# Optimization experiments

Hardware: AMD Instinct MI355X
Metric: run time of the kernel (lower is better)

## Reference

```python
import jax, jax.numpy as jnp
import numpy as np

B, N, K, IN_CH = 512, 64, 16, 6   # graphs, nodes per graph, knn, input features
EPS = 1e-5


def _w(key, shape, fan_in):
    return jax.random.normal(key, shape, jnp.float32) / np.sqrt(fan_in)


def setup_inputs() -> dict:
    key = jax.random.key(0)
    ks = jax.random.split(key, 16)
    f32 = jnp.float32
    inp = {
        "x": jax.random.normal(ks[0], (B * N, IN_CH), f32),
        "batch": (jnp.arange(B * N, dtype=jnp.int32) // N).astype(jnp.int32),
        # input projection 6 -> 64
        "w_in": _w(ks[1], (IN_CH, 64), IN_CH), "g_in": jnp.ones(64, f32), "b_in": jnp.zeros(64, f32),
        # ec1: SharedMLP([128, 64, 64])
        "w1a": _w(ks[2], (128, 64), 128), "g1a": jnp.ones(64, f32), "b1a": jnp.zeros(64, f32),
        "w1b": _w(ks[3], (64, 64), 64),   "g1b": jnp.ones(64, f32), "b1b": jnp.zeros(64, f32),
        # ec2: SharedMLP([128, 128, 128])
        "w2a": _w(ks[4], (128, 128), 128), "g2a": jnp.ones(128, f32), "b2a": jnp.zeros(128, f32),
        "w2b": _w(ks[5], (128, 128), 128), "g2b": jnp.ones(128, f32), "b2b": jnp.zeros(128, f32),
        # ec3: SharedMLP([256, 256, 256])
        "w3a": _w(ks[6], (256, 256), 256), "g3a": jnp.ones(256, f32), "b3a": jnp.zeros(256, f32),
        "w3b": _w(ks[7], (256, 256), 256), "g3b": jnp.ones(256, f32), "b3b": jnp.zeros(256, f32),
        # classifier head (dropout is identity in eval mode)
        "wc1": _w(ks[8], (896, 512), 896), "gc1": jnp.ones(512, f32), "bc1": jnp.zeros(512, f32),
        "wc2": _w(ks[9], (512, 256), 512), "gc2": jnp.ones(256, f32), "bc2": jnp.zeros(256, f32),
        "wc3": _w(ks[10], (256, 2), 256),  "bc3": jnp.zeros(2, f32),
    }
    return inp


def bn(h, g, b):
    # training-mode BatchNorm1d over all leading (node/edge) dims, biased var
    ax = tuple(range(h.ndim - 1))
    m = h.mean(ax)
    v = h.var(ax)
    return g * (h - m) * jax.lax.rsqrt(v + EPS) + b


def lrelu(h):
    return jax.nn.leaky_relu(h, 0.2)


def knn(x):
    # x: [B,N,C]; per-graph squared-Euclidean kNN (excluding self)
    sq = jnp.sum(x * x, -1)
    d = sq[:, :, None] - 2.0 * jnp.einsum('bnc,bmc->bnm', x, x) + sq[:, None, :]
    _, idx = jax.lax.top_k(-d, K + 1)  # K+1 smallest distances
    return idx[:, :, 1:]               # drop self -> [B,N,K]


def edge_conv(x, w1, g1, b1, w2, g2, b2):
    # Dynamic EdgeConv, aggr='max'. Edge (src=centre c, dst=neighbour n):
    # target x_i = x_n, message = MLP(cat[x_i, x_j - x_i]) with x_j = x_c.
    idx = knn(x)                                     # [B,N,K]
    xn = jax.vmap(lambda xb, ib: xb[ib])(x, idx)     # [B,N,K,C] neighbours
    xc = x[:, :, None, :]                            # centres broadcast
    feat = jnp.concatenate([xn, xc - xn], -1)        # [B,N,K,2C]
    h = lrelu(bn(feat @ w1, g1, b1))
    h = lrelu(bn(h @ w2, g2, b2))                    # [B,N,K,Cout]
    C = h.shape[-1]

    def scatter_max(ib, hb):  # per-graph max-scatter to destination nodes
        out = jnp.full((N, C), -jnp.inf, hb.dtype)
        return out.at[ib.reshape(-1)].max(hb.reshape(-1, C))

    res = jax.vmap(scatter_max)(idx, h)
    return jnp.where(jnp.isneginf(res), 0.0, res)    # nodes w/o in-edges -> 0


def reference(x, batch, w_in, g_in, b_in,
              w1a, g1a, b1a, w1b, g1b, b1b,
              w2a, g2a, b2a, w2b, g2b, b2b,
              w3a, g3a, b3a, w3b, g3b, b3b,
              wc1, gc1, bc1, wc2, gc2, bc2, wc3, bc3):
    # batch == arange(B*N)//N (equal-size graphs), encoded by the [B,N] reshape
    h0 = lrelu(bn(x @ w_in, g_in, b_in)).reshape(B, N, 64)
    h1 = edge_conv(h0, w1a, g1a, b1a, w1b, g1b, b1b)   # [B,N,64]
    h2 = edge_conv(h1, w2a, g2a, b2a, w2b, g2b, b2b)   # [B,N,128]
    h3 = edge_conv(h2, w3a, g3a, b3a, w3b, g3b, b3b)   # [B,N,256]
    h = jnp.concatenate([h1, h2, h3], -1)              # [B,N,448]
    pooled = jnp.concatenate([h.mean(1), h.max(1)], -1)  # [B,896]
    z = lrelu(bn(pooled @ wc1, gc1, bc1))
    z = lrelu(bn(z @ wc2, gc2, bc2))
    return z @ wc3 + bc3                               # [B,2] logits
```

## Files before the change

kernel.cpp:

```cpp
#include <hip/hip_runtime.h>
#include <hip/hip_fp16.h>
#include <math.h>

#define BB 512
#define NN 64
#define KNB 16
#define NPTS (BB*NN)
#define NEDGE (BB*NN*KNB)
#define EPSV 1e-5f

typedef __attribute__((ext_vector_type(8))) _Float16 f16x8;
typedef __attribute__((ext_vector_type(4))) _Float16 f16x4;
typedef __attribute__((ext_vector_type(4))) float f32x4;

__device__ __forceinline__ float lrelu(float x){ return fmaxf(x, 0.2f*x); }
__device__ __forceinline__ unsigned encf(float f){
    unsigned u = __float_as_uint(f);
    return (u & 0x80000000u) ? ~u : (u | 0x80000000u);
}
__device__ __forceinline__ float decf(unsigned e){
    unsigned u = (e & 0x80000000u) ? (e ^ 0x80000000u) : ~e;
    return __uint_as_float(u);
}
#define ENC_NEGINF 0x007FFFFFu

__device__ __forceinline__ float dec_ec(unsigned e, float ca, float cb, float gv){
    if (e == ENC_NEGINF) return 0.0f;
    float s = (gv < 0.0f) ? -1.0f : 1.0f;
    return lrelu(ca*(s*decf(e)) + cb);
}

__device__ __forceinline__ void split2h(float v, _Float16& h, _Float16& m){
    h = (_Float16)v;
    float r = v - (float)h;
    m = (_Float16)(r * 2048.0f);
}

__global__ void k_input(const float* __restrict__ x, const float* __restrict__ w,
                        float* __restrict__ h0){
    __shared__ float wls[6*64];
    int t = threadIdx.x;
    for (int i = t; i < 6*64; i += 256) wls[i] = w[i];
    __syncthreads();
    int row = blockIdx.x*256 + t;
    float xv[6];
#pragma unroll
    for (int k = 0; k < 6; k++) xv[k] = x[row*6 + k];
#pragma unroll 8
    for (int c = 0; c < 64; c++){
        float acc = 0.f;
#pragma unroll
        for (int k = 0; k < 6; k++) acc += xv[k]*wls[k*64 + c];
        h0[(size_t)row*64 + c] = acc;
    }
}

__global__ void k_colstats_part(const float* __restrict__ h,
                                float* __restrict__ pS, float* __restrict__ pQ){
    int t = threadIdx.x;
    int c = t & 63;
    int g = t >> 6;
    int p = blockIdx.x*4 + g;
    const int rpb = NPTS/256;
    int r0 = p*rpb;
    float s = 0.f, q = 0.f;
    for (int r = r0; r < r0 + rpb; r++){
        float v = h[(size_t)r*64 + c];
        s += v; q += v*v;
    }
    pS[c*256 + p] = s;
    pQ[c*256 + p] = q;
}

__global__ void k_bnfin_part(const float* __restrict__ pS, const float* __restrict__ pQ,
                             const float* __restrict__ g, const float* __restrict__ b,
                             float* __restrict__ cA, float* __restrict__ cB,
                             int P, float invM){
    int c = threadIdx.x;
    const float* ps = pS + (size_t)c*P;
    const float* pq = pQ + (size_t)c*P;
    float s = 0.f, q = 0.f;
    for (int p = 0; p < P; p += 4){
        float4 vs = *(const float4*)(ps + p);
        float4 vq = *(const float4*)(pq + p);
        s += vs.x + vs.y + vs.z + vs.w;
        q += vq.x + vq.y + vq.z + vq.w;
    }
    float m = s*invM;
    float v = q*invM - m*m;
    v = v < 0.f ? 0.f : v;
    float a = g[c]*rsqrtf(v + EPSV);
    cA[c] = a;
    cB[c] = b[c] - m*a;
}

__global__ void k_bnfin(const float* gs, const float* gq, const float* g,
                        const float* b, float* cA, float* cB, int C, float invM){
    int c = blockIdx.x*blockDim.x + threadIdx.x;
    if (c < C){
        float m = gs[c]*invM;
        float v = gq[c]*invM - m*m;
        v = v < 0.f ? 0.f : v;
        float a = g[c]*rsqrtf(v + EPSV);
        cA[c] = a;
        cB[c] = b[c] - m*a;
    }
}

template<int C, int MODE>
__global__ void k_knn(const void* __restrict__ xin, int* __restrict__ idxg,
                      const float* __restrict__ cA, const float* __restrict__ cB,
                      const float* __restrict__ g){
    const int CP = C + 4;
    __shared__ __align__(16) float xls[64*CP];
    __shared__ float sq[64];
    __shared__ __align__(16) float dls[64*64];
    int t = threadIdx.x, b = blockIdx.x;
    if (MODE == 0){
        const float* xb = (const float*)xin + (size_t)b*64*C;
        for (int i = t; i < 64*C; i += 256){
            int n = i / C, c = i & (C-1);
            xls[n*CP + c] = lrelu(cA[c]*xb[i] + cB[c]);
        }
    } else {
        const unsigned* xb = (const unsigned*)xin + (size_t)b*64*C;
        for (int i = t; i < 64*C; i += 256){
            int n = i / C, c = i & (C-1);
            xls[n*CP + c] = dec_ec(xb[i], cA[c], cB[c], g[c]);
        }
    }
    __syncthreads();
    if (t < 64){
        float s = 0.f;
        for (int c = 0; c < C; c += 4){
            float4 v = *(const float4*)&xls[t*CP + c];
            s += v.x*v.x + v.y*v.y + v.z*v.z + v.w*v.w;
        }
        sq[t] = s;
    }
    __syncthreads();
    {
        int n0 = (t >> 3)*2;
        int m0 = (t & 7)*8;
        float acc[2][8];
#pragma unroll
        for (int r = 0; r < 2; r++)
#pragma unroll
            for (int i = 0; i < 8; i++) acc[r][i] = 0.f;
        const float* an0 = &xls[n0*CP];
        const float* an1 = &xls[(n0+1)*CP];
        const float* bm  = &xls[m0*CP];
        for (int c = 0; c < C; c += 4){
            float4 a0 = *(const float4*)(an0 + c);
            float4 a1 = *(const float4*)(an1 + c);
#pragma unroll
            for (int i = 0; i < 8; i++){
                float4 bv = *(const float4*)(bm + i*CP + c);
                acc[0][i] += a0.x*bv.x + a0.y*bv.y + a0.z*bv.z + a0.w*bv.w;
                acc[1][i] += a1.x*bv.x + a1.y*bv.y + a1.z*bv.z + a1.w*bv.w;
            }
        }
#pragma unroll
        for (int r = 0; r < 2; r++){
            float sn = sq[n0 + r];
#pragma unroll
            for (int i4 = 0; i4 < 8; i4 += 4){
                float4 dv;
                dv.x = sn - 2.0f*acc[r][i4+0] + sq[m0+i4+0];
                dv.y = sn - 2.0f*acc[r][i4+1] + sq[m0+i4+1];
                dv.z = sn - 2.0f*acc[r][i4+2] + sq[m0+i4+2];
                dv.w = sn - 2.0f*acc[r][i4+3] + sq[m0+i4+3];
                *(float4*)&dls[(n0+r)*64 + m0 + i4] = dv;
            }
        }
    }
    __syncthreads();
    int lane = t & 63, w = t >> 6;
    for (int pr = 0; pr < 16; pr += 4){
        int n0 = w*16 + pr;
        unsigned long long c0 = (((unsigned long long)encf(dls[(n0+0)*64 + lane])) << 32) | (unsigned)lane;
        unsigned long long c1 = (((unsigned long long)encf(dls[(n0+1)*64 + lane])) << 32) | (unsigned)lane;
        unsigned long long c2 = (((unsigned long long)encf(dls[(n0+2)*64 + lane])) << 32) | (unsigned)lane;
        unsigned long long c3 = (((unsigned long long)encf(dls[(n0+3)*64 + lane])) << 32) | (unsigned)lane;
#pragma unroll
        for (int k = 2; k <= 64; k <<= 1){
#pragma unroll
            for (int j = k >> 1; j > 0; j >>= 1){
                bool keepmin = ((lane & j) == 0) == ((lane & k) == 0);
                unsigned long long o0 = __shfl_xor(c0, j, 64);
                unsigned long long o1 = __shfl_xor(c1, j, 64);
                unsigned long long o2 = __shfl_xor(c2, j, 64);
                unsigned long long o3 = __shfl_xor(c3, j, 64);
                c0 = keepmin ? (c0 < o0 ? c0 : o0) : (c0 < o0 ? o0 : c0);
                c1 = keepmin ? (c1 < o1 ? c1 : o1) : (c1 < o1 ? o1 : c1);
                c2 = keepmin ? (c2 < o2 ? c2 : o2) : (c2 < o2 ? o2 : c2);
                c3 = keepmin ? (c3 < o3 ? c3 : o3) : (c3 < o3 ? o3 : c3);
            }
        }
        if (lane >= 1 && lane <= KNB){
            int base = b*1024 + n0*16 + lane - 1;
            idxg[base]      = (int)(c0 & 0xffffffffu);
            idxg[base + 16] = (int)(c1 & 0xffffffffu);
            idxg[base + 32] = (int)(c2 & 0xffffffffu);
            idxg[base + 48] = (int)(c3 & 0xffffffffu);
        }
    }
}

__global__ void k_wprep_all(const float* __restrict__ w1a, const float* __restrict__ w2a,
                            const float* __restrict__ w3a,
                            _Float16* __restrict__ w1bh, _Float16* __restrict__ w1bm,
                            _Float16* __restrict__ w1dh, _Float16* __restrict__ w1dm,
                            _Float16* __restrict__ w2bh, _Float16* __restrict__ w2bm,
                            _Float16* __restrict__ w2dh, _Float16* __restrict__ w2dm,
                            _Float16* __restrict__ w3bh, _Float16* __restrict__ w3dh){
    int blk = blockIdx.x, t = threadIdx.x;
    if (blk < 16){
        const int CIN = 64, CMID = 64;
        int i = blk*256 + t;
        int k = i / CMID, c = i - k*CMID;
        float wb = w1a[(size_t)(CIN + k)*CMID + c];
        float wd = w1a[(size_t)k*CMID + c] - wb;
        size_t o = (size_t)c*CIN + k;
        _Float16 h, m;
        split2h(wb, h, m); w1bh[o] = h; w1bm[o] = m;
        split2h(wd, h, m); w1dh[o] = h; w1dm[o] = m;
    } else if (blk < 48){
        const int CIN = 64, CMID = 128;
        int i = (blk - 16)*256 + t;
        int k = i / CMID, c = i - k*CMID;
        float wb = w2a[(size_t)(CIN + k)*CMID + c];
        float wd = w2a[(size_t)k*CMID + c] - wb;
        size_t o = (size_t)c*CIN + k;
        _Float16 h, m;
        split2h(wb, h, m); w2bh[o] = h; w2bm[o] = m;
        split2h(wd, h, m); w2dh[o] = h; w2dm[o] = m;
    } else {
        const int CIN = 128, CMID = 256;
        int i = (blk - 48)*256 + t;
        int k = i / CMID, c = i - k*CMID;
        float wb = w3a[(size_t)(CIN + k)*CMID + c];
        float wd = w3a[(size_t)k*CMID + c] - wb;
        size_t o = (size_t)c*CIN + k;
        w3bh[o] = (_Float16)wb;
        w3dh[o] = (_Float16)wd;
    }
}

template<int CIN, int CMID, int MODE>
__global__ __launch_bounds__(256)
void k_mm1x_st(const void* __restrict__ xin,
               const float* __restrict__ cAin, const float* __restrict__ cBin,
               const float* __restrict__ gin,
               const _Float16* __restrict__ wbh, const _Float16* __restrict__ wbm,
               const _Float16* __restrict__ wdh, const _Float16* __restrict__ wdm,
               const int* __restrict__ idxg,
               float* __restrict__ P, float* __restrict__ Q,
               float* __restrict__ pS, float* __restrict__ pQ){
    const int ASP = CMID + 9;
    __shared__ float Pls[64*ASP];
    __shared__ float Qls[64*ASP];
    __shared__ int ils[1024];
    int t = threadIdx.x, b = blockIdx.x;
    int lane = t & 63, w = t >> 6;
    int lrow = lane & 15, lk = lane >> 4;
    for (int i = t; i < 1024; i += 256) ils[i] = idxg[b*1024 + i];

    const int KT = CIN/32;
    f16x8 ah[KT], am[KT];
    {
        size_t rowg = (size_t)b*64 + w*16 + lrow;
#pragma unroll
        for (int kt = 0; kt < KT; kt++){
            union { f16x8 v; _Float16 u[8]; } H, M;
#pragma unroll
            for (int j = 0; j < 8; j++){
                int k = kt*32 + lk*8 + j;
                float v;
                if (MODE == 0){
                    float raw = ((const float*)xin)[rowg*CIN + k];
                    v = lrelu(cAin[k]*raw + cBin[k]);
                } else {
                    unsigned e = ((const unsigned*)xin)[rowg*CIN + k];
                    v = dec_ec(e, cAin[k], cBin[k], gin[k]);
                }
                split2h(v, H.u[j], M.u[j]);
            }
            ah[kt] = H.v; am[kt] = M.v;
        }
    }
#pragma unroll
    for (int ct = 0; ct < CMID/16; ct++){
        int col = ct*16 + lrow;
        f32x4 aPM = {0,0,0,0}, aPC = {0,0,0,0};
        f32x4 aQM = {0,0,0,0}, aQC = {0,0,0,0};
#pragma unroll
        for (int kt = 0; kt < KT; kt++){
            size_t bo = (size_t)col*CIN + kt*32 + lk*8;
            f16x8 bbh = *(const f16x8*)(wbh + bo);
            f16x8 bbm = *(const f16x8*)(wbm + bo);
            f16x8 bdh = *(const f16x8*)(wdh + bo);
            f16x8 bdm = *(const f16x8*)(wdm + bo);
            aPM = __builtin_amdgcn_mfma_f32_16x16x32_f16(ah[kt], bbh, aPM, 0, 0, 0);
            aPC = __builtin_amdgcn_mfma_f32_16x16x32_f16(ah[kt], bbm, aPC, 0, 0, 0);
            aPC = __builtin_amdgcn_mfma_f32_16x16x32_f16(am[kt], bbh, aPC, 0, 0, 0);
            aQM = __builtin_amdgcn_mfma_f32_16x16x32_f16(ah[kt], bdh, aQM, 0, 0, 0);
            aQC = __builtin_amdgcn_mfma_f32_16x16x32_f16(ah[kt], bdm, aQC, 0, 0, 0);
            aQC = __builtin_amdgcn_mfma_f32_16x16x32_f16(am[kt], bdh, aQC, 0, 0, 0);
        }
#pragma unroll
        for (int u = 0; u < 4; u++){
            int row = w*16 + lk*4 + u;
            size_t o = ((size_t)b*64 + row)*CMID + col;
            float pv = aPM[u] + aPC[u]*(1.0f/2048.0f);
            float qv = aQM[u] + aQC[u]*(1.0f/2048.0f);
            P[o] = pv; Q[o] = qv;
            Pls[row*ASP + col] = pv;
            Qls[row*ASP + col] = qv;
        }
    }
    __syncthreads();
    {
        const int NG = 256/CMID;
        const int PT = 512*NG;
        const int NPG = 64/NG;
        int c  = t & (CMID-1);
        int gg = t / CMID;
        float s = 0.f, q = 0.f;
        for (int n = gg*NPG; n < (gg+1)*NPG; n++){
            float p = Pls[n*ASP + c];
#pragma unroll 4
            for (int k = 0; k < 16; k++){
                int j = ils[n*16 + k];
                float v = p + Qls[j*ASP + c];
                s += v; q += v*v;
            }
        }
        int p = b*NG + gg;
        pS[(size_t)c*PT + p] = s;
        pQ[(size_t)c*PT + p] = q;
    }
}

template<int CIN, int CMID>
__global__ __launch_bounds__(256)
void k_mm1xh_st(const unsigned* __restrict__ xin,
                const float* __restrict__ cAin, const float* __restrict__ cBin,
                const float* __restrict__ gin,
                const _Float16* __restrict__ wbh, const _Float16* __restrict__ wdh,
                const int* __restrict__ idxg,
                _Float16* __restrict__ P, _Float16* __restrict__ Q,
                float* __restrict__ pS, float* __restrict__ pQ){
    const int ASP = CMID + 9;
    __shared__ _Float16 Pls[64*ASP];
    __shared__ _Float16 Qls[64*ASP];
    __shared__ int ils[1024];
    int t = threadIdx.x, b = blockIdx.x;
    int lane = t & 63, w = t >> 6;
    int lrow = lane & 15, lk = lane >> 4;
    for (int i = t; i < 1024; i += 256) ils[i] = idxg[b*1024 + i];

    const int KT = CIN/32;
    f16x8 ah[KT];
    {
        size_t rowg = (size_t)b*64 + w*16 + lrow;
#pragma unroll
        for (int kt = 0; kt < KT; kt++){
            union { f16x8 v; _Float16 u[8]; } H;
#pragma unroll
            for (int j = 0; j < 8; j++){
                int k = kt*32 + lk*8 + j;
                unsigned e = xin[rowg*CIN + k];
                H.u[j] = (_Float16)dec_ec(e, cAin[k], cBin[k], gin[k]);
            }
            ah[kt] = H.v;
        }
    }
#pragma unroll
    for (int ct = 0; ct < CMID/16; ct++){
        int col = ct*16 + lrow;
        f32x4 aP = {0,0,0,0}, aQ = {0,0,0,0};
#pragma unroll
        for (int kt = 0; kt < KT; kt++){
            size_t bo = (size_t)col*CIN + kt*32 + lk*8;
            f16x8 bbh = *(const f16x8*)(wbh + bo);
            f16x8 bdh = *(const f16x8*)(wdh + bo);
            aP = __builtin_amdgcn_mfma_f32_16x16x32_f16(ah[kt], bbh, aP, 0, 0, 0);
            aQ = __builtin_amdgcn_mfma_f32_16x16x32_f16(ah[kt], bdh, aQ, 0, 0, 0);
        }
#pragma unroll
        for (int u = 0; u < 4; u++){
            int row = w*16 + lk*4 + u;
            size_t o = ((size_t)b*64 + row)*CMID + col;
            _Float16 hp = (_Float16)aP[u];
            _Float16 hq = (_Float16)aQ[u];
            P[o] = hp; Q[o] = hq;
            Pls[row*ASP + col] = hp;
            Qls[row*ASP + col] = hq;
        }
    }
    __syncthreads();
    {
        float s = 0.f, q = 0.f;
        for (int n = 0; n < 64; n++){
            float p = (float)Pls[n*ASP + t];
#pragma unroll 4
            for (int k = 0; k < 16; k++){
                int j = ils[n*16 + k];
                float v = p + (float)Qls[j*ASP + t];
                s += v; q += v*v;
            }
        }
        pS[(size_t)t*512 + b] = s;
        pQ[(size_t)t*512 + b] = q;
    }
}

template<int CMID, int COUT, int NSET>
__global__ __launch_bounds__(256, 3)
void k_mm2s(const float* __restrict__ P, const float* __restrict__ Q,
            const int* __restrict__ idxg,
            const float* __restrict__ cA1, const float* __restrict__ cB1,
            const float* __restrict__ w2, const float* __restrict__ g2,
            unsigned* __restrict__ outenc,
            float* __restrict__ pS, float* __restrict__ pQ){
    const int AS = CMID + 8;
    const int NCOL = 64*NSET;
    const int NM = CMID/32;
    __shared__ __align__(16) _Float16 act_h[32*AS];
    __shared__ __align__(16) _Float16 act_m[32*AS];
    __shared__ unsigned maxtab[NCOL*65];
    __shared__ __align__(4) unsigned char ils8[1024];
    int t = threadIdx.x, b = blockIdx.x, cc = blockIdx.y;
    int lane = t & 63, w = t >> 6;
    int lrow = lane & 15, lk = lane >> 4;

    for (int i = t; i < 1024; i += 256) ils8[i] = (unsigned char)idxg[b*1024 + i];
    for (int i = t; i < NCOL*65; i += 256) maxtab[i] = ENC_NEGINF;

    int kq  = (t*4) & (CMID-1);
    int le0 = (t*4) / CMID;
    int PH  = (le0*NM) >> 4;
    float4 caq = *(const float4*)(cA1 + kq);
    float4 cbq = *(const float4*)(cB1 + kq);

    const int KT = CMID/32;
    f16x8 bh[NSET][KT], bm[NSET][KT];
    float sg[NSET];
    int ccBase = cc*NCOL;
#pragma unroll
    for (int s = 0; s < NSET; s++){
        int ncol = ccBase + s*64 + w*16 + lrow;
#pragma unroll
        for (int kt = 0; kt < KT; kt++){
            union { f16x8 v; _Float16 u[8]; } uh, um;
#pragma unroll
            for (int j = 0; j < 8; j++){
                int k = kt*32 + lk*8 + j;
                split2h(w2[(size_t)k*COUT + ncol], uh.u[j], um.u[j]);
            }
// ... 212 lines not shown
        for (int r = 0; r < 2; r++)
#pragma unroll
            for (int s = 0; s < NSET; s++) acc[r][s] = {0.f,0.f,0.f,0.f};
        __builtin_amdgcn_s_setprio(1);
#pragma unroll
        for (int kt = 0; kt < KT; kt++){
            int ko = kt*32 + lk*8;
#pragma unroll
            for (int r = 0; r < 2; r++){
                f16x8 a = *(const f16x8*)&act[(r*16 + lrow)*AS + ko];
#pragma unroll
                for (int s = 0; s < NSET; s++)
                    acc[r][s] = __builtin_amdgcn_mfma_f32_16x16x32_f16(a, breg[s][kt], acc[r][s], 0, 0, 0);
            }
        }
        __builtin_amdgcn_s_setprio(0);
#pragma unroll
        for (int r = 0; r < 2; r++){
#pragma unroll
            for (int s = 0; s < NSET; s++){
#pragma unroll
                for (int u = 0; u < 4; u++){
                    float v = acc[r][s][u];
                    ss[s] += v; qq[s] += v*v;
                    int colL = s*64 + w*16 + lrow;
                    atomicMax(&maxtab[colL*65 + jj[r][u]], encf(sg[s]*v));
                }
            }
        }
        __syncthreads();
    }
#pragma unroll
    for (int s = 0; s < NSET; s++){
        ss[s] += __shfl_xor(ss[s], 16, 64); ss[s] += __shfl_xor(ss[s], 32, 64);
        qq[s] += __shfl_xor(qq[s], 16, 64); qq[s] += __shfl_xor(qq[s], 32, 64);
        if (lane < 16){
            pS[(size_t)(ccBase + s*64 + w*16 + lane)*512 + b] = ss[s];
            pQ[(size_t)(ccBase + s*64 + w*16 + lane)*512 + b] = qq[s];
        }
    }
    for (int i = t; i < 64*NCOL; i += 256){
        int colL = i % NCOL, j = i / NCOL;
        outenc[((size_t)b*64 + j)*COUT + ccBase + colL] = maxtab[colL*65 + j];
    }
}

__global__ void k_pool(const unsigned* __restrict__ h1e, const unsigned* __restrict__ h2e,
                       const unsigned* __restrict__ h3e,
                       const float* __restrict__ cA1, const float* __restrict__ cB1,
                       const float* __restrict__ g1,
                       const float* __restrict__ cA2, const float* __restrict__ cB2,
                       const float* __restrict__ g2,
                       const float* __restrict__ cA3, const float* __restrict__ cB3,
                       const float* __restrict__ g3,
                       float* __restrict__ pooled){
    int t = threadIdx.x, b = blockIdx.x;
    for (int c = t; c < 448; c += 256){
        const unsigned* p; int C; float ca, cb, gv;
        if (c < 64){        p = h1e + (size_t)b*64*64  + c;        C = 64;  ca = cA1[c];     cb = cB1[c];     gv = g1[c]; }
        else if (c < 192){  p = h2e + (size_t)b*64*128 + (c-64);   C = 128; ca = cA2[c-64];  cb = cB2[c-64];  gv = g2[c-64]; }
        else {              p = h3e + (size_t)b*64*256 + (c-192);  C = 256; ca = cA3[c-192]; cb = cB3[c-192]; gv = g3[c-192]; }
        float s = 0.f, mx = -INFINITY;
        for (int n = 0; n < 64; n++){
            float v = dec_ec(p[(size_t)n*C], ca, cb, gv);
            s += v; mx = fmaxf(mx, v);
        }
        pooled[b*896 + c] = s*(1.0f/64.0f);
        pooled[b*896 + 448 + c] = mx;
    }
}

__global__ void k_fc1(const float* __restrict__ pooled, const float* __restrict__ w,
                      float* __restrict__ z, float* gs, float* gq){
    int r = blockIdx.x;
    int co = blockIdx.y*256 + threadIdx.x;
    const float* pr = pooled + r*896;
    float acc = 0.f;
    for (int k = 0; k < 896; k++) acc += pr[k]*w[(size_t)k*512 + co];
    z[(size_t)r*512 + co] = acc;
    atomicAdd(&gs[co], acc);
    atomicAdd(&gq[co], acc*acc);
}

__global__ void k_fc2(const float* __restrict__ z1, const float* __restrict__ cA,
                      const float* __restrict__ cB, const float* __restrict__ w,
                      float* __restrict__ z2, float* gs, float* gq){
    int r = blockIdx.x;
    int co = threadIdx.x;
    const float* zr = z1 + (size_t)r*512;
    float acc = 0.f;
    for (int k = 0; k < 512; k++){
        float v = lrelu(cA[k]*zr[k] + cB[k]);
        acc += v*w[(size_t)k*256 + co];
    }
    z2[(size_t)r*256 + co] = acc;
    atomicAdd(&gs[co], acc);
    atomicAdd(&gq[co], acc*acc);
}

__global__ void k_fc3(const float* __restrict__ z2, const float* __restrict__ cA,
                      const float* __restrict__ cB, const float* __restrict__ w,
                      const float* __restrict__ bias, float* __restrict__ out){
    int r = blockIdx.x*256 + threadIdx.x;
    const float* zr = z2 + (size_t)r*256;
    float a0 = 0.f, a1 = 0.f;
    for (int k = 0; k < 256; k++){
        float v = lrelu(cA[k]*zr[k] + cB[k]);
        a0 += v*w[k*2 + 0];
        a1 += v*w[k*2 + 1];
    }
    out[r*2 + 0] = a0 + bias[0];
    out[r*2 + 1] = a1 + bias[1];
}

extern "C" void kernel_launch(void* const* d_in, const int* in_sizes, int n_in,
                              void* d_out, int out_size, void* d_ws, size_t ws_size,
                              hipStream_t stream){
    const float* x    = (const float*)d_in[0];
    const float* w_in = (const float*)d_in[2];
    const float* g_in = (const float*)d_in[3];
    const float* b_in = (const float*)d_in[4];
    const float* w1a  = (const float*)d_in[5];
    const float* g1a  = (const float*)d_in[6];
    const float* b1a  = (const float*)d_in[7];
    const float* w1b  = (const float*)d_in[8];
    const float* g1b  = (const float*)d_in[9];
    const float* b1b  = (const float*)d_in[10];
    const float* w2a  = (const float*)d_in[11];
    const float* g2a  = (const float*)d_in[12];
    const float* b2a  = (const float*)d_in[13];
    const float* w2b  = (const float*)d_in[14];
    const float* g2b  = (const float*)d_in[15];
    const float* b2b  = (const float*)d_in[16];
    const float* w3a  = (const float*)d_in[17];
    const float* g3a  = (const float*)d_in[18];
    const float* b3a  = (const float*)d_in[19];
    const float* w3b  = (const float*)d_in[20];
    const float* g3b  = (const float*)d_in[21];
    const float* b3b  = (const float*)d_in[22];
    const float* wc1  = (const float*)d_in[23];
    const float* gc1  = (const float*)d_in[24];
    const float* bc1  = (const float*)d_in[25];
    const float* wc2  = (const float*)d_in[26];
    const float* gc2  = (const float*)d_in[27];
    const float* bc2  = (const float*)d_in[28];
    const float* wc3  = (const float*)d_in[29];
    const float* bc3  = (const float*)d_in[30];

    char* ws = (char*)d_ws;
    size_t off = 0;
    auto alloc = [&](size_t bytes){
        size_t o = off; off = (off + bytes + 255) & ~(size_t)255; return o;
    };
    float* h0     = (float*)(ws + alloc((size_t)NPTS*64*4));
    float* h1     = (float*)(ws + alloc((size_t)NPTS*64*4));
    float* h2     = (float*)(ws + alloc((size_t)NPTS*128*4));
    float* h3     = (float*)(ws + alloc((size_t)NPTS*256*4));
    float* P      = (float*)(ws + alloc((size_t)NPTS*256*4));
    float* Q      = (float*)(ws + alloc((size_t)NPTS*256*4));
    int*   idx    = (int*)  (ws + alloc((size_t)NPTS*16*4));
    float* pooled = (float*)(ws + alloc((size_t)512*896*4));
    float* z1     = (float*)(ws + alloc((size_t)512*512*4));
    float* z2     = (float*)(ws + alloc((size_t)512*256*4));
    float* pS     = (float*)(ws + alloc((size_t)131072*4));
    float* pQ     = (float*)(ws + alloc((size_t)131072*4));
    float* stats  = (float*)(ws + alloc((size_t)2048*4));
    float* coefs  = (float*)(ws + alloc((size_t)3456*4));
    _Float16* wsp = (_Float16*)(ws + alloc((size_t)114688*2));

    _Float16 *w1bh = wsp,          *w1bm = wsp+4096,
             *w1dh = wsp+8192,     *w1dm = wsp+12288;
    _Float16 *w2bh = wsp+16384,    *w2bm = wsp+24576,
             *w2dh = wsp+32768,    *w2dm = wsp+40960;
    _Float16 *w3bh = wsp+49152,    *w3dh = wsp+81920;

    float *f1s  = stats,       *f1q  = stats+512;
    float *f2s  = stats+1024,  *f2q  = stats+1280;
    float *cA0   = coefs,      *cB0   = coefs+64;
    float *cA1a  = coefs+128,  *cB1a  = coefs+192;
    float *cA1b  = coefs+256,  *cB1b  = coefs+320;
    float *cA2a  = coefs+384,  *cB2a  = coefs+512;
    float *cA2b  = coefs+640,  *cB2b  = coefs+768;
    float *cA3a  = coefs+896,  *cB3a  = coefs+1152;
    float *cA3b  = coefs+1408, *cB3b  = coefs+1664;
    float *cAf1  = coefs+1920, *cBf1  = coefs+2432;
    float *cAf2  = coefs+2944, *cBf2  = coefs+3200;

    (void)hipMemsetAsync(stats, 0, 2048*4, stream);

    k_wprep_all<<<176, 256, 0, stream>>>(w1a, w2a, w3a,
                                         w1bh, w1bm, w1dh, w1dm,
                                         w2bh, w2bm, w2dh, w2dm,
                                         w3bh, w3dh);

    k_input<<<NPTS/256, 256, 0, stream>>>(x, w_in, h0);
    k_colstats_part<<<64, 256, 0, stream>>>(h0, pS, pQ);
    k_bnfin_part<<<1, 64, 0, stream>>>(pS, pQ, g_in, b_in, cA0, cB0, 256, 1.0f/NPTS);

    k_knn<64,0><<<BB, 256, 0, stream>>>(h0, idx, cA0, cB0, nullptr);
    k_mm1x_st<64,64,0><<<BB, 256, 0, stream>>>(h0, cA0, cB0, nullptr,
                                               w1bh, w1bm, w1dh, w1dm, idx,
                                               P, Q, pS, pQ);
    k_bnfin_part<<<1, 64, 0, stream>>>(pS, pQ, g1a, b1a, cA1a, cB1a, 2048, 1.0f/NEDGE);
    k_mm2s<64,64,1><<<dim3(BB,1), 256, 0, stream>>>(P, Q, idx, cA1a, cB1a, w1b, g1b,
                                                    (unsigned*)h1, pS, pQ);
    k_bnfin_part<<<1, 64, 0, stream>>>(pS, pQ, g1b, b1b, cA1b, cB1b, 512, 1.0f/NEDGE);

    k_knn<64,1><<<BB, 256, 0, stream>>>(h1, idx, cA1b, cB1b, g1b);
    k_mm1x_st<64,128,1><<<BB, 256, 0, stream>>>(h1, cA1b, cB1b, g1b,
                                                w2bh, w2bm, w2dh, w2dm, idx,
                                                P, Q, pS, pQ);
    k_bnfin_part<<<1, 128, 0, stream>>>(pS, pQ, g2a, b2a, cA2a, cB2a, 1024, 1.0f/NEDGE);
    k_mm2s<128,128,2><<<dim3(BB,1), 256, 0, stream>>>(P, Q, idx, cA2a, cB2a, w2b, g2b,
                                                      (unsigned*)h2, pS, pQ);
    k_bnfin_part<<<1, 128, 0, stream>>>(pS, pQ, g2b, b2b, cA2b, cB2b, 512, 1.0f/NEDGE);

    k_knn<128,1><<<BB, 256, 0, stream>>>(h2, idx, cA2b, cB2b, g2b);
    k_mm1xh_st<128,256><<<BB, 256, 0, stream>>>((const unsigned*)h2, cA2b, cB2b, g2b,
                                                w3bh, w3dh, idx,
                                                (_Float16*)P, (_Float16*)Q, pS, pQ);
    k_bnfin_part<<<1, 256, 0, stream>>>(pS, pQ, g3a, b3a, cA3a, cB3a, 512, 1.0f/NEDGE);
    k_mm2xh<256,256,2><<<dim3(BB,2), 256, 0, stream>>>((_Float16*)P, (_Float16*)Q, idx,
                                                       cA3a, cB3a, w3b, g3b,
                                                       (unsigned*)h3, pS, pQ);
    k_bnfin_part<<<1, 256, 0, stream>>>(pS, pQ, g3b, b3b, cA3b, cB3b, 512, 1.0f/NEDGE);

    k_pool<<<BB, 256, 0, stream>>>((const unsigned*)h1, (const unsigned*)h2,
                                   (const unsigned*)h3,
                                   cA1b, cB1b, g1b, cA2b, cB2b, g2b, cA3b, cB3b, g3b,
                                   pooled);
    k_fc1<<<dim3(512,2), 256, 0, stream>>>(pooled, wc1, z1, f1s, f1q);
    k_bnfin<<<2, 256, 0, stream>>>(f1s, f1q, gc1, bc1, cAf1, cBf1, 512, 1.0f/512);
    k_fc2<<<512, 256, 0, stream>>>(z1, cAf1, cBf1, wc2, z2, f2s, f2q);
    k_bnfin<<<1, 256, 0, stream>>>(f2s, f2q, gc2, bc2, cAf2, cBf2, 256, 1.0f/512);
    k_fc3<<<2, 256, 0, stream>>>(z2, cAf2, cBf2, wc3, bc3, (float*)d_out);

    (void)in_sizes; (void)n_in; (void)out_size; (void)ws_size;
}
```

Measured before the change: 1.042 ms.

## Fuse kNN into first edge-conv matmul kernels and fold FC BN finalize

The separate kNN kernel is merged into the first-stage edge-conv matmul kernels. The decoded features are kept in shared memory, where they feed both the distance computation and the A-operand fragments, and the neighbour indices go straight to shared memory as well as global. This removes a kernel launch per layer, the re-read and re-decode of the input features, and the index reload. It also folds the classifier BN finalize into the fc2/fc3 kernels, so two tiny launches disappear. The costs are a union shared buffer with an extra barrier, possibly higher shared-memory use per block, and redundant per-block recomputation of BN coefficients in fc2.

```diff
diff --git a/kernel.cpp b/kernel.cpp
--- a/kernel.cpp
+++ b/kernel.cpp
@@ -92,119 +92,6 @@
     float a = g[c]*rsqrtf(v + EPSV);
     cA[c] = a;
     cB[c] = b[c] - m*a;
-}
-
-__global__ void k_bnfin(const float* gs, const float* gq, const float* g,
-                        const float* b, float* cA, float* cB, int C, float invM){
-    int c = blockIdx.x*blockDim.x + threadIdx.x;
-    if (c < C){
-        float m = gs[c]*invM;
-        float v = gq[c]*invM - m*m;
-        v = v < 0.f ? 0.f : v;
-        float a = g[c]*rsqrtf(v + EPSV);
-        cA[c] = a;
-        cB[c] = b[c] - m*a;
-    }
-}
-
-template<int C, int MODE>
-__global__ void k_knn(const void* __restrict__ xin, int* __restrict__ idxg,
-                      const float* __restrict__ cA, const float* __restrict__ cB,
-                      const float* __restrict__ g){
-    const int CP = C + 4;
-    __shared__ __align__(16) float xls[64*CP];
-    __shared__ float sq[64];
-    __shared__ __align__(16) float dls[64*64];
-    int t = threadIdx.x, b = blockIdx.x;
-    if (MODE == 0){
-        const float* xb = (const float*)xin + (size_t)b*64*C;
-        for (int i = t; i < 64*C; i += 256){
-            int n = i / C, c = i & (C-1);
-            xls[n*CP + c] = lrelu(cA[c]*xb[i] + cB[c]);
-        }
-    } else {
-        const unsigned* xb = (const unsigned*)xin + (size_t)b*64*C;
-        for (int i = t; i < 64*C; i += 256){
-            int n = i / C, c = i & (C-1);
-            xls[n*CP + c] = dec_ec(xb[i], cA[c], cB[c], g[c]);
-        }
-    }
-    __syncthreads();
-    if (t < 64){
-        float s = 0.f;
-        for (int c = 0; c < C; c += 4){
-            float4 v = *(const float4*)&xls[t*CP + c];
-            s += v.x*v.x + v.y*v.y + v.z*v.z + v.w*v.w;
-        }
-        sq[t] = s;
-    }
-    __syncthreads();
-    {
-        int n0 = (t >> 3)*2;
-        int m0 = (t & 7)*8;
-        float acc[2][8];
-#pragma unroll
-        for (int r = 0; r < 2; r++)
-#pragma unroll
-            for (int i = 0; i < 8; i++) acc[r][i] = 0.f;
-        const float* an0 = &xls[n0*CP];
-        const float* an1 = &xls[(n0+1)*CP];
-        const float* bm  = &xls[m0*CP];
-        for (int c = 0; c < C; c += 4){
-            float4 a0 = *(const float4*)(an0 + c);
-            float4 a1 = *(const float4*)(an1 + c);
-#pragma unroll
-            for (int i = 0; i < 8; i++){
-                float4 bv = *(const float4*)(bm + i*CP + c);
-                acc[0][i] += a0.x*bv.x + a0.y*bv.y + a0.z*bv.z + a0.w*bv.w;
-                acc[1][i] += a1.x*bv.x + a1.y*bv.y + a1.z*bv.z + a1.w*bv.w;
-            }
-        }
-#pragma unroll
-        for (int r = 0; r < 2; r++){
-            float sn = sq[n0 + r];
-#pragma unroll
-            for (int i4 = 0; i4 < 8; i4 += 4){
-                float4 dv;
-                dv.x = sn - 2.0f*acc[r][i4+0] + sq[m0+i4+0];
-                dv.y = sn - 2.0f*acc[r][i4+1] + sq[m0+i4+1];
-                dv.z = sn - 2.0f*acc[r][i4+2] + sq[m0+i4+2];
-                dv.w = sn - 2.0f*acc[r][i4+3] + sq[m0+i4+3];
-                *(float4*)&dls[(n0+r)*64 + m0 + i4] = dv;
-            }
-        }
-    }
-    __syncthreads();
-    int lane = t & 63, w = t >> 6;
-    for (int pr = 0; pr < 16; pr += 4){
-        int n0 = w*16 + pr;
-        unsigned long long c0 = (((unsigned long long)encf(dls[(n0+0)*64 + lane])) << 32) | (unsigned)lane;
-        unsigned long long c1 = (((unsigned long long)encf(dls[(n0+1)*64 + lane])) << 32) | (unsigned)lane;
-        unsigned long long c2 = (((unsigned long long)encf(dls[(n0+2)*64 + lane])) << 32) | (unsigned)lane;
-        unsigned long long c3 = (((unsigned long long)encf(dls[(n0+3)*64 + lane])) << 32) | (unsigned)lane;
-#pragma unroll
-        for (int k = 2; k <= 64; k <<= 1){
-#pragma unroll
-            for (int j = k >> 1; j > 0; j >>= 1){
-                bool keepmin = ((lane & j) == 0) == ((lane & k) == 0);
-                unsigned long long o0 = __shfl_xor(c0, j, 64);
-                unsigned long long o1 = __shfl_xor(c1, j, 64);
-                unsigned long long o2 = __shfl_xor(c2, j, 64);
-                unsigned long long o3 = __shfl_xor(c3, j, 64);
-                c0 = keepmin ? (c0 < o0 ? c0 : o0) : (c0 < o0 ? o0 : c0);
-                c1 = keepmin ? (c1 < o1 ? c1 : o1) : (c1 < o1 ? o1 : c1);
-                c2 = keepmin ? (c2 < o2 ? c2 : o2) : (c2 < o2 ? o2 : c2);
-                c3 = keepmin ? (c3 < o3 ? c3 : o3) : (c3 < o3 ? o3 : c3);
-            }
-        }
-        if (lane >= 1 && lane <= KNB){
-            int base = b*1024 + n0*16 + lane - 1;
-            idxg[base]      = (int)(c0 & 0xffffffffu);
-            idxg[base + 16] = (int)(c1 & 0xffffffffu);
-            idxg[base + 32] = (int)(c2 & 0xffffffffu);
-            idxg[base + 48] = (int)(c3 & 0xffffffffu);
-        }
-    }
 }
 
 __global__ void k_wprep_all(const float* __restrict__ w1a, const float* __restrict__ w2a,
@@ -249,46 +136,138 @@
 
 template<int CIN, int CMID, int MODE>
 __global__ __launch_bounds__(256)
-void k_mm1x_st(const void* __restrict__ xin,
-               const float* __restrict__ cAin, const float* __restrict__ cBin,
-               const float* __restrict__ gin,
-               const _Float16* __restrict__ wbh, const _Float16* __restrict__ wbm,
-               const _Float16* __restrict__ wdh, const _Float16* __restrict__ wdm,
-               const int* __restrict__ idxg,
-               float* __restrict__ P, float* __restrict__ Q,
-               float* __restrict__ pS, float* __restrict__ pQ){
+void k_ec1(const void* __restrict__ xin,
+           const float* __restrict__ cA, const float* __restrict__ cB,
+           const float* __restrict__ g,
+           const _Float16* __restrict__ wbh, const _Float16* __restrict__ wbm,
+           const _Float16* __restrict__ wdh, const _Float16* __restrict__ wdm,
+           int* __restrict__ idxg,
+           float* __restrict__ P, float* __restrict__ Q,
+           float* __restrict__ pS, float* __restrict__ pQ){
+    const int CP  = CIN + 4;
     const int ASP = CMID + 9;
-    __shared__ float Pls[64*ASP];
-    __shared__ float Qls[64*ASP];
+    constexpr int BA = 64*(CIN+4)*4 + 64*64*4 + 64*4;
+    constexpr int BBY = 2*64*(CMID+9)*4;
+    constexpr int UB = (BA > BBY) ? BA : BBY;
+    __shared__ __align__(16) char ubuf[UB];
     __shared__ int ils[1024];
+    float* xls = (float*)ubuf;
+    float* dls = (float*)(ubuf + (size_t)64*CP*4);
+    float* sq  = (float*)(ubuf + (size_t)64*CP*4 + (size_t)64*64*4);
+    float* Pls = (float*)ubuf;
+    float* Qls = (float*)(ubuf + (size_t)64*ASP*4);
+
     int t = threadIdx.x, b = blockIdx.x;
     int lane = t & 63, w = t >> 6;
     int lrow = lane & 15, lk = lane >> 4;
-    for (int i = t; i < 1024; i += 256) ils[i] = idxg[b*1024 + i];
-
+
+    if (MODE == 0){
+        const float* xb = (const float*)xin + (size_t)b*64*CIN;
+        for (int i = t; i < 64*CIN; i += 256){
+            int n = i / CIN, c = i & (CIN-1);
+            xls[n*CP + c] = lrelu(cA[c]*xb[i] + cB[c]);
+        }
+    } else {
+        const unsigned* xb = (const unsigned*)xin + (size_t)b*64*CIN;
+        for (int i = t; i < 64*CIN; i += 256){
+            int n = i / CIN, c = i & (CIN-1);
+            xls[n*CP + c] = dec_ec(xb[i], cA[c], cB[c], g[c]);
+        }
+    }
+    __syncthreads();
+    if (t < 64){
+        float s = 0.f;
+        for (int c = 0; c < CIN; c += 4){
+            float4 v = *(const float4*)&xls[t*CP + c];
+            s += v.x*v.x + v.y*v.y + v.z*v.z + v.w*v.w;
+        }
+        sq[t] = s;
+    }
+    __syncthreads();
+    {
+        int n0 = (t >> 3)*2;
+        int m0 = (t & 7)*8;
+        float acc[2][8];
+#pragma unroll
+        for (int r = 0; r < 2; r++)
+#pragma unroll
+            for (int i = 0; i < 8; i++) acc[r][i] = 0.f;
+        const float* an0 = &xls[n0*CP];
+        const float* an1 = &xls[(n0+1)*CP];
+        const float* bm  = &xls[m0*CP];
+        for (int c = 0; c < CIN; c += 4){
+            float4 a0 = *(const float4*)(an0 + c);
+            float4 a1 = *(const float4*)(an1 + c);
+#pragma unroll
+            for (int i = 0; i < 8; i++){
+                float4 bv = *(const float4*)(bm + i*CP + c);
+                acc[0][i] += a0.x*bv.x + a0.y*bv.y + a0.z*bv.z + a0.w*bv.w;
+                acc[1][i] += a1.x*bv.x + a1.y*bv.y + a1.z*bv.z + a1.w*bv.w;
+            }
+        }
+#pragma unroll
+        for (int r = 0; r < 2; r++){
+            float sn = sq[n0 + r];
+#pragma unroll
+            for (int i4 = 0; i4 < 8; i4 += 4){
+                float4 dv;
+                dv.x = sn - 2.0f*acc[r][i4+0] + sq[m0+i4+0];
+                dv.y = sn - 2.0f*acc[r][i4+1] + sq[m0+i4+1];
+                dv.z = sn - 2.0f*acc[r][i4+2] + sq[m0+i4+2];
+                dv.w = sn - 2.0f*acc[r][i4+3] + sq[m0+i4+3];
+                *(float4*)&dls[(n0+r)*64 + m0 + i4] = dv;
+            }
+        }
+    }
+    __syncthreads();
+    for (int pr = 0; pr < 16; pr += 4){
+        int n0 = w*16 + pr;
+        unsigned long long c0 = (((unsigned long long)encf(dls[(n0+0)*64 + lane])) << 32) | (unsigned)lane;
+        unsigned long long c1 = (((unsigned long long)encf(dls[(n0+1)*64 + lane])) << 32) | (unsigned)lane;
+        unsigned long long c2 = (((unsigned long long)encf(dls[(n0+2)*64 + lane])) << 32) | (unsigned)lane;
+        unsigned long long c3 = (((unsigned long long)encf(dls[(n0+3)*64 + lane])) << 32) | (unsigned)lane;
+#pragma unroll
+        for (int k = 2; k <= 64; k <<= 1){
+#pragma unroll
+            for (int j = k >> 1; j > 0; j >>= 1){
+                bool keepmin = ((lane & j) == 0) == ((lane & k) == 0);
+                unsigned long long o0 = __shfl_xor(c0, j, 64);
+                unsigned long long o1 = __shfl_xor(c1, j, 64);
+                unsigned long long o2 = __shfl_xor(c2, j, 64);
+                unsigned long long o3 = __shfl_xor(c3, j, 64);
+                c0 = keepmin ? (c0 < o0 ? c0 : o0) : (c0 < o0 ? o0 : c0);
+                c1 = keepmin ? (c1 < o1 ? c1 : o1) : (c1 < o1 ? o1 : c1);
+                c2 = keepmin ? (c2 < o2 ? c2 : o2) : (c2 < o2 ? o2 : c2);
+                c3 = keepmin ? (c3 < o3 ? c3 : o3) : (c3 < o3 ? o3 : c3);
+            }
+        }
+        if (lane >= 1 && lane <= KNB){
+            int lb = n0*16 + lane - 1;
+            int base = b*1024 + lb;
+            int v0 = (int)(c0 & 0xffffffffu);
+            int v1 = (int)(c1 & 0xffffffffu);
+            int v2 = (int)(c2 & 0xffffffffu);
+            int v3 = (int)(c3 & 0xffffffffu);
+            idxg[base]      = v0; ils[lb]      = v0;
+            idxg[base + 16] = v1; ils[lb + 16] = v1;
+            idxg[base + 32] = v2; ils[lb + 32] = v2;
+            idxg[base + 48] = v3; ils[lb + 48] = v3;
+        }
+    }
     const int KT = CIN/32;
     f16x8 ah[KT], am[KT];
     {
-        size_t rowg = (size_t)b*64 + w*16 + lrow;
+        const float* xr = &xls[(w*16 + lrow)*CP];
 #pragma unroll
         for (int kt = 0; kt < KT; kt++){
             union { f16x8 v; _Float16 u[8]; } H, M;
 #pragma unroll
-            for (int j = 0; j < 8; j++){
-                int k = kt*32 + lk*8 + j;
-                float v;
-                if (MODE == 0){
-                    float raw = ((const float*)xin)[rowg*CIN + k];
-                    v = lrelu(cAin[k]*raw + cBin[k]);
-                } else {
-                    unsigned e = ((const unsigned*)xin)[rowg*CIN + k];
-                    v = dec_ec(e, cAin[k], cBin[k], gin[k]);
-                }
-                split2h(v, H.u[j], M.u[j]);
-            }
+            for (int j = 0; j < 8; j++)
+                split2h(xr[kt*32 + lk*8 + j], H.u[j], M.u[j]);
             ah[kt] = H.v; am[kt] = M.v;
         }
     }
+    __syncthreads();
 #pragma unroll
     for (int ct = 0; ct < CMID/16; ct++){
         int col = ct*16 + lrow;
@@ -344,38 +323,131 @@
 
 template<int CIN, int CMID>
 __global__ __launch_bounds__(256)
-void k_mm1xh_st(const unsigned* __restrict__ xin,
-                const float* __restrict__ cAin, const float* __restrict__ cBin,
-                const float* __restrict__ gin,
-                const _Float16* __restrict__ wbh, const _Float16* __restrict__ wdh,
-                const int* __restrict__ idxg,
-                _Float16* __restrict__ P, _Float16* __restrict__ Q,
-                float* __restrict__ pS, float* __restrict__ pQ){
+void k_ec1h(const unsigned* __restrict__ xin,
+            const float* __restrict__ cA, const float* __restrict__ cB,
+            const float* __restrict__ g,
+            const _Float16* __restrict__ wbh, const _Float16* __restrict__ wdh,
+            int* __restrict__ idxg,
+            _Float16* __restrict__ P, _Float16* __restrict__ Q,
+            float* __restrict__ pS, float* __restrict__ pQ){
+    const int CP  = CIN + 4;
     const int ASP = CMID + 9;
-    __shared__ _Float16 Pls[64*ASP];
-    __shared__ _Float16 Qls[64*ASP];
+    constexpr int BA = 64*(CIN+4)*4 + 64*64*4 + 64*4;
+    constexpr int BBY = 2*64*(CMID+9)*2;
+    constexpr int UB = (BA > BBY) ? BA : BBY;
+    __shared__ __align__(16) char ubuf[UB];
     __shared__ int ils[1024];
+    float* xls = (float*)ubuf;
+    float* dls = (float*)(ubuf + (size_t)64*CP*4);
+    float* sq  = (float*)(ubuf + (size_t)64*CP*4 + (size_t)64*64*4);
+    _Float16* Pls = (_Float16*)ubuf;
+    _Float16* Qls = (_Float16*)(ubuf + (size_t)64*ASP*2);
+
     int t = threadIdx.x, b = blockIdx.x;
     int lane = t & 63, w = t >> 6;
     int lrow = lane & 15, lk = lane >> 4;
-    for (int i = t; i < 1024; i += 256) ils[i] = idxg[b*1024 + i];
-
+
+    {
+        const unsigned* xb = xin + (size_t)b*64*CIN;
+        for (int i = t; i < 64*CIN; i += 256){
+            int n = i / CIN, c = i & (CIN-1);
+            xls[n*CP + c] = dec_ec(xb[i], cA[c], cB[c], g[c]);
+        }
+    }
+    __syncthreads();
+    if (t < 64){
+        float s = 0.f;
+        for (int c = 0; c < CIN; c += 4){
+            float4 v = *(const float4*)&xls[t*CP + c];
+            s += v.x*v.x + v.y*v.y + v.z*v.z + v.w*v.w;
+        }
+        sq[t] = s;
+    }
+    __syncthreads();
+    {
+        int n0 = (t >> 3)*2;
+        int m0 = (t & 7)*8;
+        float acc[2][8];
+#pragma unroll
+        for (int r = 0; r < 2; r++)
+#pragma unroll
+            for (int i = 0; i < 8; i++) acc[r][i] = 0.f;
+        const float* an0 = &xls[n0*CP];
+        const float* an1 = &xls[(n0+1)*CP];
+        const float* bm  = &xls[m0*CP];
+        for (int c = 0; c < CIN; c += 4){
+            float4 a0 = *(const float4*)(an0 + c);
+            float4 a1 = *(const float4*)(an1 + c);
+#pragma unroll
+            for (int i = 0; i < 8; i++){
+                float4 bv = *(const float4*)(bm + i*CP + c);
+                acc[0][i] += a0.x*bv.x + a0.y*bv.y + a0.z*bv.z + a0.w*bv.w;
+                acc[1][i] += a1.x*bv.x + a1.y*bv.y + a1.z*bv.z + a1.w*bv.w;
+            }
+        }
+#pragma unroll
+        for (int r = 0; r < 2; r++){
+            float sn = sq[n0 + r];
+#pragma unroll
+            for (int i4 = 0; i4 < 8; i4 += 4){
+                float4 dv;
+                dv.x = sn - 2.0f*acc[r][i4+0] + sq[m0+i4+0];
+                dv.y = sn - 2.0f*acc[r][i4+1] + sq[m0+i4+1];
+                dv.z = sn - 2.0f*acc[r][i4+2] + sq[m0+i4+2];
+                dv.w = sn - 2.0f*acc[r][i4+3] + sq[m0+i4+3];
+                *(float4*)&dls[(n0+r)*64 + m0 + i4] = dv;
+            }
+        }
+    }
+    __syncthreads();
+    for (int pr = 0; pr < 16; pr += 4){
+        int n0 = w*16 + pr;
+        unsigned long long c0 = (((unsigned long long)encf(dls[(n0+0)*64 + lane])) << 32) | (unsigned)lane;
+        unsigned long long c1 = (((unsigned long long)encf(dls[(n0+1)*64 + lane])) << 32) | (unsigned)lane;
+        unsigned long long c2 = (((unsigned long long)encf(dls[(n0+2)*64 + lane])) << 32) | (unsigned)lane;
+        unsigned long long c3 = (((unsigned long long)encf(dls[(n0+3)*64 + lane])) << 32) | (unsigned)lane;
+#pragma unroll
+        for (int k = 2; k <= 64; k <<= 1){
+#pragma unroll
+            for (int j = k >> 1; j > 0; j >>= 1){
+                bool keepmin = ((lane & j) == 0) == ((lane & k) == 0);
+                unsigned long long o0 = __shfl_xor(c0, j, 64);
+                unsigned long long o1 = __shfl_xor(c1, j, 64);
+                unsigned long long o2 = __shfl_xor(c2, j, 64);
+                unsigned long long o3 = __shfl_xor(c3, j, 64);
+                c0 = keepmin ? (c0 < o0 ? c0 : o0) : (c0 < o0 ? o0 : c0);
+                c1 = keepmin ? (c1 < o1 ? c1 : o1) : (c1 < o1 ? o1 : c1);
+                c2 = keepmin ? (c2 < o2 ? c2 : o2) : (c2 < o2 ? o2 : c2);
+                c3 = keepmin ? (c3 < o3 ? c3 : o3) : (c3 < o3 ? o3 : c3);
+            }
+        }
+        if (lane >= 1 && lane <= KNB){
+            int lb = n0*16 + lane - 1;
+            int base = b*1024 + lb;
+            int v0 = (int)(c0 & 0xffffffffu);
+            int v1 = (int)(c1 & 0xffffffffu);
+            int v2 = (int)(c2 & 0xffffffffu);
+            int v3 = (int)(c3 & 0xffffffffu);
+            idxg[base]      = v0; ils[lb]      = v0;
+            idxg[base + 16] = v1; ils[lb + 16] = v1;
+            idxg[base + 32] = v2; ils[lb + 32] = v2;
+            idxg[base + 48] = v3; ils[lb + 48] = v3;
+        }
+    }
     const int KT = CIN/32;
     f16x8 ah[KT];
     {
-        size_t rowg = (size_t)b*64 + w*16 + lrow;
+        const float* xr = &xls[(w*16 + lrow)*CP];
 #pragma unroll
         for (int kt = 0; kt < KT; kt++){
             union { f16x8 v; _Float16 u[8]; } H;
 #pragma unroll
-            for (int j = 0; j < 8; j++){
-                int k = kt*32 + lk*8 + j;
-                unsigned e = xin[rowg*CIN + k];
-                H.u[j] = (_Float16)dec_ec(e, cAin[k], cBin[k], gin[k]);
-            }
+            for (int j = 0; j < 8; j++)
+                H.u[j] = (_Float16)xr[kt*32 + lk*8 + j];
             ah[kt] = H.v;
         }
     }
+    __syncthreads();
 #pragma unroll
     for (int ct = 0; ct < CMID/16; ct++){
         int col = ct*16 + lrow;
@@ -754,15 +826,27 @@
     atomicAdd(&gq[co], acc*acc);
 }
 
-__global__ void k_fc2(const float* __restrict__ z1, const float* __restrict__ cA,
-                      const float* __restrict__ cB, const float* __restrict__ w,
+__global__ void k_fc2(const float* __restrict__ z1,
+                      const float* __restrict__ gs1, const float* __restrict__ gq1,
+                      const float* __restrict__ g, const float* __restrict__ bb,
+                      const float* __restrict__ w,
                       float* __restrict__ z2, float* gs, float* gq){
+    __shared__ float cAl[512], cBl[512];
+    for (int c = threadIdx.x; c < 512; c += 256){
+        float m = gs1[c]*(1.0f/512);
+        float v = gq1[c]*(1.0f/512) - m*m;
+        v = v < 0.f ? 0.f : v;
+        float a = g[c]*rsqrtf(v + EPSV);
+        cAl[c] = a;
+        cBl[c] = bb[c] - m*a;
+    }
+    __syncthreads();
     int r = blockIdx.x;
     int co = threadIdx.x;
     const float* zr = z1 + (size_t)r*512;
     float acc = 0.f;
     for (int k = 0; k < 512; k++){
-        float v = lrelu(cA[k]*zr[k] + cB[k]);
+        float v = lrelu(cAl[k]*zr[k] + cBl[k]);
         acc += v*w[(size_t)k*256 + co];
     }
     z2[(size_t)r*256 + co] = acc;
@@ -770,14 +854,27 @@
     atomicAdd(&gq[co], acc*acc);
 }
 
-__global__ void k_fc3(const float* __restrict__ z2, const float* __restrict__ cA,
-                      const float* __restrict__ cB, const float* __restrict__ w,
+__global__ void k_fc3(const float* __restrict__ z2,
+                      const float* __restrict__ gs2, const float* __restrict__ gq2,
+                      const float* __restrict__ g, const float* __restrict__ bb,
+                      const float* __restrict__ w,
                       const float* __restrict__ bias, float* __restrict__ out){
+    __shared__ float cAl[256], cBl[256];
+    {
+        int c = threadIdx.x;
+        float m = gs2[c]*(1.0f/512);
+        float v = gq2[c]*(1.0f/512) - m*m;
+        v = v < 0.f ? 0.f : v;
+        float a = g[c]*rsqrtf(v + EPSV);
+        cAl[c] = a;
+        cBl[c] = bb[c] - m*a;
+    }
+    __syncthreads();
     int r = blockIdx.x*256 + threadIdx.x;
     const float* zr = z2 + (size_t)r*256;
     float a0 = 0.f, a1 = 0.f;
     for (int k = 0; k < 256; k++){
-        float v = lrelu(cA[k]*zr[k] + cB[k]);
+        float v = lrelu(cAl[k]*zr[k] + cBl[k]);
         a0 += v*w[k*2 + 0];
         a1 += v*w[k*2 + 1];
     }
@@ -855,8 +952,6 @@
     float *cA2b  = coefs+640,  *cB2b  = coefs+768;
     float *cA3a  = coefs+896,  *cB3a  = coefs+1152;
     float *cA3b  = coefs+1408, *cB3b  = coefs+1664;
-    float *cAf1  = coefs+1920, *cBf1  = coefs+2432;
-    float *cAf2  = coefs+2944, *cBf2  = coefs+3200;
 
     (void)hipMemsetAsync(stats, 0, 2048*4, stream);
 
@@ -869,28 +964,25 @@
     k_colstats_part<<<64, 256, 0, stream>>>(h0, pS, pQ);
     k_bnfin_part<<<1, 64, 0, stream>>>(pS, pQ, g_in, b_in, cA0, cB0, 256, 1.0f/NPTS);
 
-    k_knn<64,0><<<BB, 256, 0, stream>>>(h0, idx, cA0, cB0, nullptr);
-    k_mm1x_st<64,64,0><<<BB, 256, 0, stream>>>(h0, cA0, cB0, nullptr,
-                                               w1bh, w1bm, w1dh, w1dm, idx,
-                                               P, Q, pS, pQ);
+    k_ec1<64,64,0><<<BB, 256, 0, stream>>>(h0, cA0, cB0, nullptr,
+                                           w1bh, w1bm, w1dh, w1dm, idx,
+                                           P, Q, pS, pQ);
     k_bnfin_part<<<1, 64, 0, stream>>>(pS, pQ, g1a, b1a, cA1a, cB1a, 2048, 1.0f/NEDGE);
     k_mm2s<64,64,1><<<dim3(BB,1), 256, 0, stream>>>(P, Q, idx, cA1a, cB1a, w1b, g1b,
                                                     (unsigned*)h1, pS, pQ);
     k_bnfin_part<<<1, 64, 0, stream>>>(pS, pQ, g1b, b1b, cA1b, cB1b, 512, 1.0f/NEDGE);
 
-    k_knn<64,1><<<BB, 256, 0, stream>>>(h1, idx, cA1b, cB1b, g1b);
-    k_mm1x_st<64,128,1><<<BB, 256, 0, stream>>>(h1, cA1b, cB1b, g1b,
-                                                w2bh, w2bm, w2dh, w2dm, idx,
-                                                P, Q, pS, pQ);
+    k_ec1<64,128,1><<<BB, 256, 0, stream>>>(h1, cA1b, cB1b, g1b,
+                                            w2bh, w2bm, w2dh, w2dm, idx,
+                                            P, Q, pS, pQ);
     k_bnfin_part<<<1, 128, 0, stream>>>(pS, pQ, g2a, b2a, cA2a, cB2a, 1024, 1.0f/NEDGE);
     k_mm2s<128,128,2><<<dim3(BB,1), 256, 0, stream>>>(P, Q, idx, cA2a, cB2a, w2b, g2b,
                                                       (unsigned*)h2, pS, pQ);
     k_bnfin_part<<<1, 128, 0, stream>>>(pS, pQ, g2b, b2b, cA2b, cB2b, 512, 1.0f/NEDGE);
 
-    k_knn<128,1><<<BB, 256, 0, stream>>>(h2, idx, cA2b, cB2b, g2b);
-    k_mm1xh_st<128,256><<<BB, 256, 0, stream>>>((const unsigned*)h2, cA2b, cB2b, g2b,
-                                                w3bh, w3dh, idx,
-                                                (_Float16*)P, (_Float16*)Q, pS, pQ);
+    k_ec1h<128,256><<<BB, 256, 0, stream>>>((const unsigned*)h2, cA2b, cB2b, g2b,
+                                            w3bh, w3dh, idx,
+                                            (_Float16*)P, (_Float16*)Q, pS, pQ);
     k_bnfin_part<<<1, 256, 0, stream>>>(pS, pQ, g3a, b3a, cA3a, cB3a, 512, 1.0f/NEDGE);
     k_mm2xh<256,256,2><<<dim3(BB,2), 256, 0, stream>>>((_Float16*)P, (_Float16*)Q, idx,
                                                        cA3a, cB3a, w3b, g3b,
@@ -902,10 +994,8 @@
                                    cA1b, cB1b, g1b, cA2b, cB2b, g2b, cA3b, cB3b, g3b,
                                    pooled);
     k_fc1<<<dim3(512,2), 256, 0, stream>>>(pooled, wc1, z1, f1s, f1q);
-    k_bnfin<<<2, 256, 0, stream>>>(f1s, f1q, gc1, bc1, cAf1, cBf1, 512, 1.0f/512);
-    k_fc2<<<512, 256, 0, stream>>>(z1, cAf1, cBf1, wc2, z2, f2s, f2q);
-    k_bnfin<<<1, 256, 0, stream>>>(f2s, f2q, gc2, bc2, cAf2, cBf2, 256, 1.0f/512);
-    k_fc3<<<2, 256, 0, stream>>>(z2, cAf2, cBf2, wc3, bc3, (float*)d_out);
+    k_fc2<<<512, 256, 0, stream>>>(z1, f1s, f1q, gc1, bc1, wc2, z2, f2s, f2q);
+    k_fc3<<<2, 256, 0, stream>>>(z2, f2s, f2q, gc2, bc2, wc3, bc3, (float*)d_out);
 
     (void)in_sizes; (void)n_in; (void)out_size; (void)ws_size;
 }
```

Result: faster. 1.009 ms (-3.2%).
